# Kernel optimization log

Measured on AMD Instinct MI355X. Metric: run time of the kernel, lower is better.

The kernel has to match this reference:

```python
import jax, jax.numpy as jnp
import numpy as np

V, D, H, L, T_CTX = 50257, 768, 12, 12, 1024
HD = D // H
GELU_C = float(np.sqrt(2.0 / np.pi))


def new_gelu(x):
    return 0.5 * x * (1.0 + jnp.tanh(GELU_C * (x + 0.044715 * x ** 3)))


def layernorm(x, w, b, eps=1e-5):
    mu = jnp.mean(x, axis=-1, keepdims=True)
    var = jnp.var(x, axis=-1, keepdims=True)
    return (x - mu) * jax.lax.rsqrt(var + eps) * w + b


def setup_inputs() -> dict:
    key = jax.random.key(0)
    ks = jax.random.split(key, 20)
    B, T = 2, 1024
    s = 0.02
    inp = {
        "idx": jax.random.randint(ks[0], (B, T), 0, V),
        "targets": jax.random.randint(ks[1], (B, T), 0, V),
        "wte": jax.random.normal(ks[2], (V, D), jnp.float32) * s,
        "wpe": jax.random.normal(ks[3], (T_CTX, D), jnp.float32) * s,
        "ln1_w": jnp.ones((L, D)), "ln1_b": jnp.zeros((L, D)),
        "qkv_w": jax.random.normal(ks[4], (L, D, 3 * D), jnp.float32) * s,
        "qkv_b": jnp.zeros((L, 3 * D)),
        "proj_w": jax.random.normal(ks[5], (L, D, D), jnp.float32) * s,
        "proj_b": jnp.zeros((L, D)),
        "ln2_w": jnp.ones((L, D)), "ln2_b": jnp.zeros((L, D)),
        "fc_w": jax.random.normal(ks[6], (L, D, 4 * D), jnp.float32) * s,
        "fc_b": jnp.zeros((L, 4 * D)),
        "fc2_w": jax.random.normal(ks[7], (L, 4 * D, D), jnp.float32) * s,
        "fc2_b": jnp.zeros((L, D)),
        "lnf_w": jnp.ones((D,)), "lnf_b": jnp.zeros((D,)),
    }
    return inp


def _gpt_forward(idx, targets, wte, wpe, ln1_w, ln1_b, qkv_w, qkv_b, proj_w,
                 proj_b, ln2_w, ln2_b, fc_w, fc_b, fc2_w, fc2_b, lnf_w, lnf_b):
    B, T = idx.shape
    x = wte[idx] + wpe[:T]  # [B,T,D]
    scale = 1.0 / np.sqrt(HD)
    causal = jnp.tril(jnp.ones((T, T), dtype=bool))

    def block(x, p):
        l1w, l1b, qw, qb, pw, pb, l2w, l2b, fw, fb, f2w, f2b = p
        h = layernorm(x, l1w, l1b)
        qkv = h @ qw + qb  # [B,T,3D]
        q, k, v = jnp.split(qkv, 3, axis=-1)
        q = q.reshape(B, T, H, HD).transpose(0, 2, 1, 3)
        k = k.reshape(B, T, H, HD).transpose(0, 2, 1, 3)
        v = v.reshape(B, T, H, HD).transpose(0, 2, 1, 3)
        attn = jnp.einsum('bhqd,bhkd->bhqk', q, k) * scale
        attn = jnp.where(causal, attn, -jnp.inf)
        attn = jax.nn.softmax(attn, axis=-1)
        o = jnp.einsum('bhqk,bhkd->bhqd', attn, v)
        o = o.transpose(0, 2, 1, 3).reshape(B, T, D)
        x = x + (o @ pw + pb)
        h = layernorm(x, l2w, l2b)
        h = new_gelu(h @ fw + fb) @ f2w + f2b
        return x + h, None

    params = (ln1_w, ln1_b, qkv_w, qkv_b, proj_w, proj_b,
              ln2_w, ln2_b, fc_w, fc_b, fc2_w, fc2_b)
    x, _ = jax.lax.scan(block, x, params)
    x = layernorm(x, lnf_w, lnf_b)
    logits = x @ wte.T  # tied lm_head, [B,T,V]

    logp = jax.nn.log_softmax(logits, axis=-1)
    tflat = targets.reshape(-1)
    valid = tflat != -1
    tsafe = jnp.where(valid, tflat, 0)
    nll = -jnp.take_along_axis(logp.reshape(-1, V), tsafe[:, None], axis=-1)[:, 0]
    loss = jnp.sum(jnp.where(valid, nll, 0.0)) / jnp.maximum(jnp.sum(valid), 1)
    return logits, loss


def reference(idx, targets, wte, wpe, ln1_w, ln1_b, qkv_w, qkv_b, proj_w,
              proj_b, ln2_w, ln2_b, fc_w, fc_b, fc2_w, fc2_b, lnf_w, lnf_b):
    return _gpt_forward(idx, targets, wte, wpe, ln1_w, ln1_b, qkv_w, qkv_b,
                        proj_w, proj_b, ln2_w, ln2_b, fc_w, fc_b, fc2_w, fc2_b,
                        lnf_w, lnf_b)
```

## Files before the change

kernel.cpp:

```cpp
#include <hip/hip_runtime.h>
#include <hip/hip_bf16.h>
#include <math.h>

#define TT 1024
#define BB 2
#define DD 768
#define HH 12
#define NHD 64
#define LL 12
#define VV 50257
#define MROWS (BB*TT)
#define VPAD 50304

typedef __attribute__((ext_vector_type(4))) float f32x4;
typedef __attribute__((ext_vector_type(8))) __bf16 bf16x8;
typedef __attribute__((ext_vector_type(8))) unsigned short u16x8;
typedef __hip_bfloat16 bf16;

__device__ __forceinline__ void gload_lds16(const bf16* g, bf16* l) {
    __builtin_amdgcn_global_load_lds((const __attribute__((address_space(1))) void*)g,
                                     (__attribute__((address_space(3))) void*)l, 16, 0, 0);
}

__global__ void embed_kernel(const int* __restrict__ idx, const float* __restrict__ wte,
                             const float* __restrict__ wpe, float* __restrict__ x) {
    int m = blockIdx.x;
    int t = m % TT;
    int tok = idx[m];
    const float* wrow = wte + (size_t)tok * DD;
    const float* prow = wpe + (size_t)t * DD;
    float* xrow = x + (size_t)m * DD;
    for (int c = threadIdx.x; c < DD; c += blockDim.x)
        xrow[c] = wrow[c] + prow[c];
}

__global__ void ln_kernel(const float* __restrict__ x, const float* __restrict__ w,
                          const float* __restrict__ b, bf16* __restrict__ out) {
    __shared__ float red[256];
    int m = blockIdx.x;
    int tid = threadIdx.x;
    const float* xr = x + (size_t)m * DD;
    float v0 = xr[tid], v1 = xr[tid + 256], v2 = xr[tid + 512];
    red[tid] = v0 + v1 + v2;
    __syncthreads();
    for (int s = 128; s > 0; s >>= 1) { if (tid < s) red[tid] += red[tid + s]; __syncthreads(); }
    float mu = red[0] * (1.0f / DD);
    __syncthreads();
    float d0 = v0 - mu, d1 = v1 - mu, d2 = v2 - mu;
    red[tid] = d0 * d0 + d1 * d1 + d2 * d2;
    __syncthreads();
    for (int s = 128; s > 0; s >>= 1) { if (tid < s) red[tid] += red[tid + s]; __syncthreads(); }
    float rstd = rsqrtf(red[0] * (1.0f / DD) + 1e-5f);
    bf16* orow = out + (size_t)m * DD;
    orow[tid]       = __float2bfloat16(d0 * rstd * w[tid]       + b[tid]);
    orow[tid + 256] = __float2bfloat16(d1 * rstd * w[tid + 256] + b[tid + 256]);
    orow[tid + 512] = __float2bfloat16(d2 * rstd * w[tid + 512] + b[tid + 512]);
}

__global__ void cast_kernel(const float* __restrict__ src, bf16* __restrict__ dst, int n4) {
    int stride = gridDim.x * blockDim.x;
    for (int i = blockIdx.x * blockDim.x + threadIdx.x; i < n4; i += stride) {
        float4 v = *(const float4*)(src + (size_t)i * 4);
        bf16* d = dst + (size_t)i * 4;
        d[0] = __float2bfloat16(v.x); d[1] = __float2bfloat16(v.y);
        d[2] = __float2bfloat16(v.z); d[3] = __float2bfloat16(v.w);
    }
}

__global__ void tcast_kernel(const float* __restrict__ W, bf16* __restrict__ Wt,
                             int K, int N, size_t wstride, size_t tstride) {
    W  += (size_t)blockIdx.z * wstride;
    Wt += (size_t)blockIdx.z * tstride;
    __shared__ float t[32][33];
    int n0 = blockIdx.x * 32, k0 = blockIdx.y * 32;
    int c = threadIdx.x & 31, g = threadIdx.x >> 5;
    #pragma unroll
    for (int i = 0; i < 4; ++i) {
        int k = g * 4 + i;
        t[k][c] = W[(size_t)(k0 + k) * N + n0 + c];
    }
    __syncthreads();
    #pragma unroll
    for (int i = 0; i < 4; ++i) {
        int n = g * 4 + i;
        Wt[(size_t)(n0 + n) * K + k0 + c] = __float2bfloat16(t[c][n]);
    }
}

template<int BM, int BN, bool BIAS, bool GELU_, bool RES, bool OUTBF16, bool NCHECK>
__global__ __launch_bounds__(256, 3) void mgemm(
        const bf16* __restrict__ A, const bf16* __restrict__ Bm,
        const float* __restrict__ bias, const float* __restrict__ res,
        float* __restrict__ Cf, bf16* __restrict__ Cb, int M, int N, int K) {
    constexpr int WM = BM / 32, WN = BN / 32;
    constexpr int RA = BM / 64, RB = BN / 64;
    constexpr int NL = RA + RB;
    __shared__ __align__(16) bf16 As[3][BM * 32];
    __shared__ __align__(16) bf16 Bs[3][BN * 32];
    const int tid = threadIdx.x, lane = tid & 63, wid = tid >> 6;
    const int nbx = gridDim.x;
    const int nwg = nbx * gridDim.y;
    const int bidl = blockIdx.x + nbx * blockIdx.y;
    const int cpx = nwg >> 3;
    const int sw = (bidl & 7) * cpx + (bidl >> 3);
    const int m0 = (sw % nbx) * BM, n0 = (sw / nbx) * BN;
    const int wr = (wid >> 1) * (BM / 2), wc = (wid & 1) * (BN / 2);
    const int fr = lane & 15, fq = lane >> 4;

    const int ksrc = ((lane & 3) ^ ((lane >> 3) & 3)) * 8;
    const bf16* gA = A  + (size_t)(m0 + wid * 16 + (lane >> 2)) * K + ksrc;
    const bf16* gB = Bm + (size_t)(n0 + wid * 16 + (lane >> 2)) * K + ksrc;
    const int kph = (fq ^ ((fr >> 1) & 3)) * 8;

    const int nt = K / 32;
    auto stage = [&](int tile) {
        bf16* dA = &As[tile % 3][0] + wid * 512 + lane * 8;
        bf16* dB = &Bs[tile % 3][0] + wid * 512 + lane * 8;
        const bf16* pA = gA + tile * 32;
        const bf16* pB = gB + tile * 32;
        #pragma unroll
        for (int i = 0; i < RA; ++i) gload_lds16(pA + (size_t)(i * 64) * K, dA + i * 2048);
        #pragma unroll
        for (int i = 0; i < RB; ++i) gload_lds16(pB + (size_t)(i * 64) * K, dB + i * 2048);
    };

    f32x4 acc[WM][WN] = {};
    stage(0);
    if (nt > 1) stage(1);

    for (int t = 0; t < nt; ++t) {
        if (t + 2 < nt) stage(t + 2);
        const int rem = nt - 1 - t;
        if (rem >= 2)      asm volatile("s_waitcnt vmcnt(%0)" :: "i"(2 * NL) : "memory");
        else if (rem == 1) asm volatile("s_waitcnt vmcnt(%0)" :: "i"(NL) : "memory");
        else               asm volatile("s_waitcnt vmcnt(0)" ::: "memory");
        __builtin_amdgcn_s_barrier();
        __builtin_amdgcn_sched_barrier(0);
        const bf16* abase = &As[t % 3][0];
        const bf16* bbase = &Bs[t % 3][0];
        bf16x8 af[WM], bq[WN];
        #pragma unroll
        for (int m = 0; m < WM; ++m)
            af[m] = *(const bf16x8*)(abase + (wr + m * 16 + fr) * 32 + kph);
        #pragma unroll
        for (int n = 0; n < WN; ++n)
            bq[n] = *(const bf16x8*)(bbase + (wc + n * 16 + fr) * 32 + kph);
        #pragma unroll
        for (int m = 0; m < WM; ++m)
            #pragma unroll
            for (int n = 0; n < WN; ++n)
                acc[m][n] = __builtin_amdgcn_mfma_f32_16x16x32_bf16(af[m], bq[n], acc[m][n], 0, 0, 0);
        __builtin_amdgcn_sched_barrier(0);
        __builtin_amdgcn_s_barrier();
    }

    #pragma unroll
    for (int m = 0; m < WM; ++m) {
        const int row = m0 + wr + m * 16 + fq * 4;
        #pragma unroll
        for (int n = 0; n < WN; ++n) {
            const int col = n0 + wc + n * 16 + fr;
            if (NCHECK && col >= N) continue;
            float bv = BIAS ? bias[col] : 0.f;
            #pragma unroll
            for (int r = 0; r < 4; ++r) {
                float v = acc[m][n][r] + bv;
                if (GELU_) {
                    float u = v;
                    v = 0.5f * u * (1.0f + tanhf(0.7978845608028654f * (u + 0.044715f * u * u * u)));
                }
                if (RES) v += res[(size_t)(row + r) * N + col];
                if (OUTBF16) Cb[(size_t)(row + r) * N + col] = __float2bfloat16(v);
                else         Cf[(size_t)(row + r) * N + col] = v;
            }
        }
    }
}

__global__ __launch_bounds__(256) void attn3_kernel(const bf16* __restrict__ qkv,
                                                    bf16* __restrict__ out) {
    __shared__ bf16 Vt[64 * 64];
    __shared__ bf16 Ps[4][16 * 64];
    const int bid = blockIdx.x;
    const int q0 = (bid % (TT / 64)) * 64;
    const int h  = (bid / (TT / 64)) % HH;
    const int b  = bid / ((TT / 64) * HH);
    const int tid = threadIdx.x, lane = tid & 63, wid = tid >> 6;
    const int fr = lane & 15, fq = lane >> 4;
    const size_t rs = 3 * DD;

    bf16x8 qf[2];
    {
        const bf16* qb = qkv + (size_t)(b * TT + q0 + wid * 16 + fr) * rs + h * NHD;
        qf[0] = *(const bf16x8*)(qb + fq * 8);
        qf[1] = *(const bf16x8*)(qb + 32 + fq * 8);
    }
    float mrun[4] = {-1e30f, -1e30f, -1e30f, -1e30f};
    float lrun[4] = {0.f, 0.f, 0.f, 0.f};
    f32x4 o[4] = {};
    const int vrow = (tid & 31) * 2, kq = tid >> 5;
    const int ntile = q0 / 64 + 1;

    for (int jt = 0; jt < ntile; ++jt) {
        __syncthreads();
        {
            const u16x8* vb = (const u16x8*)(qkv + (size_t)(b * TT + jt * 64 + vrow) * rs + 2 * DD + h * NHD + kq * 8);
            u16x8 v0 = vb[0];
            u16x8 v1 = *(const u16x8*)((const bf16*)vb + rs);
            #pragma unroll
            for (int j = 0; j < 8; ++j) {
                int d = kq * 8 + j;
                int e = (d * 64 + vrow) ^ ((d & 7) << 3);
                *(unsigned int*)&Vt[e] = (unsigned int)v0[j] | ((unsigned int)v1[j] << 16);
            }
        }
        f32x4 s[4] = {};
        const bf16* kb = qkv + (size_t)(b * TT + jt * 64 + fr) * rs + DD + h * NHD;
        #pragma unroll
        for (int n = 0; n < 4; ++n) {
            bf16x8 k0 = *(const bf16x8*)(kb + (size_t)(n * 16) * rs + fq * 8);
            bf16x8 k1 = *(const bf16x8*)(kb + (size_t)(n * 16) * rs + 32 + fq * 8);
            s[n] = __builtin_amdgcn_mfma_f32_16x16x32_bf16(qf[0], k0, s[n], 0, 0, 0);
            s[n] = __builtin_amdgcn_mfma_f32_16x16x32_bf16(qf[1], k1, s[n], 0, 0, 0);
        }
        float mt[4] = {-1e30f, -1e30f, -1e30f, -1e30f};
        #pragma unroll
        for (int n = 0; n < 4; ++n) {
            int colg = jt * 64 + n * 16 + fr;
            #pragma unroll
            for (int r = 0; r < 4; ++r) {
                int rowg = q0 + wid * 16 + fq * 4 + r;
                float v = s[n][r] * 0.125f;
                if (colg > rowg) v = -1e30f;
                s[n][r] = v;
                mt[r] = fmaxf(mt[r], v);
            }
        }
        #pragma unroll
        for (int msk = 1; msk <= 8; msk <<= 1)
            #pragma unroll
            for (int r = 0; r < 4; ++r) mt[r] = fmaxf(mt[r], __shfl_xor(mt[r], msk));
        float sc[4], pt[4] = {0.f, 0.f, 0.f, 0.f};
        #pragma unroll
        for (int r = 0; r < 4; ++r) {
            float mn = fmaxf(mrun[r], mt[r]);
            sc[r] = __expf(mrun[r] - mn);
            mrun[r] = mn;
        }
        #pragma unroll
        for (int n = 0; n < 4; ++n)
            #pragma unroll
            for (int r = 0; r < 4; ++r) {
                float p = __expf(s[n][r] - mrun[r]);
                s[n][r] = p;
                pt[r] += p;
            }
        #pragma unroll
        for (int msk = 1; msk <= 8; msk <<= 1)
            #pragma unroll
            for (int r = 0; r < 4; ++r) pt[r] += __shfl_xor(pt[r], msk);
        #pragma unroll
        for (int r = 0; r < 4; ++r) lrun[r] = lrun[r] * sc[r] + pt[r];
        #pragma unroll
        for (int n2 = 0; n2 < 4; ++n2)
            #pragma unroll
            for (int r = 0; r < 4; ++r) o[n2][r] *= sc[r];
        #pragma unroll
        for (int n = 0; n < 4; ++n)
            #pragma unroll
            for (int r = 0; r < 4; ++r) {
                int row = fq * 4 + r;
                int e = (row * 64 + n * 16 + fr) ^ ((row & 7) << 3);
                Ps[wid][e] = __float2bfloat16(s[n][r]);
            }
        __syncthreads();
        #pragma unroll
        for (int ks = 0; ks < 2; ++ks) {
            int pe = (fr * 64 + ks * 32 + fq * 8) ^ ((fr & 7) << 3);
            bf16x8 pa = *(const bf16x8*)&Ps[wid][pe];
            #pragma unroll
            for (int n2 = 0; n2 < 4; ++n2) {
                int d = n2 * 16 + fr;
                int ve = (d * 64 + ks * 32 + fq * 8) ^ ((d & 7) << 3);
                bf16x8 vv = *(const bf16x8*)&Vt[ve];
                o[n2] = __builtin_amdgcn_mfma_f32_16x16x32_bf16(pa, vv, o[n2], 0, 0, 0);
            }
        }
    }
    #pragma unroll
    for (int r = 0; r < 4; ++r) {
        float inv = 1.f / lrun[r];
        bf16* op = out + (size_t)(b * TT + q0 + wid * 16 + fq * 4 + r) * DD + h * NHD;
        #pragma unroll
        for (int n2 = 0; n2 < 4; ++n2)
            op[n2 * 16 + fr] = __float2bfloat16(o[n2][r] * inv);
    }
}

__global__ void zero_kernel(float* p) { if (threadIdx.x == 0) p[0] = 0.f; }

__device__ __forceinline__ void ol_push(float v, float& mx, float& sm) {
    if (v > mx) { sm *= __expf(mx - v); mx = v; }
    sm += __expf(v - mx);
}

__global__ void loss_kernel(const float* __restrict__ logits, const int* __restrict__ targets,
                            float* __restrict__ acc) {
    __shared__ float rm[256], rs[256];
    int m = blockIdx.x;
    int tid = threadIdx.x;
    const float* lr = logits + (size_t)m * VV;
    const int lead = (4 - (m & 3)) & 3;
    const int nv = (VV - lead) >> 2;
    float mx = -1e30f, sm = 0.f;
    if (tid < lead) ol_push(lr[tid], mx, sm);
    const float4* lr4 = (const float4*)(lr + lead);
    for (int i = tid; i < nv; i += 256) {
        float4 v = lr4[i];
        ol_push(v.x, mx, sm); ol_push(v.y, mx, sm);
        ol_push(v.z, mx, sm); ol_push(v.w, mx, sm);
    }
    for (int i = lead + 4 * nv + tid; i < VV; i += 256) ol_push(lr[i], mx, sm);
    rm[tid] = mx; rs[tid] = sm;
    __syncthreads();
    for (int s = 128; s > 0; s >>= 1) {
        if (tid < s) {
            float m2 = rm[tid + s], s2 = rs[tid + s];
            float nm = fmaxf(rm[tid], m2);
            rs[tid] = rs[tid] * __expf(rm[tid] - nm) + s2 * __expf(m2 - nm);
            rm[tid] = nm;
        }
        __syncthreads();
    }
    if (tid == 0) {
        float lse = logf(rs[0]) + rm[0];
        atomicAdd(acc, lse - lr[targets[m]]);
    }
}

__global__ void loss_final(const float* __restrict__ acc, float* __restrict__ out) {
    if (threadIdx.x == 0) out[0] = acc[0] * (1.0f / (float)MROWS);
}

extern "C" void kernel_launch(void* const* d_in, const int* in_sizes, int n_in,
                              void* d_out, int out_size, void* d_ws, size_t ws_size,
                              hipStream_t stream) {
    const int*   idx     = (const int*)d_in[0];
    const int*   targets = (const int*)d_in[1];
    const float* wte     = (const float*)d_in[2];
    const float* wpe     = (const float*)d_in[3];
    const float* ln1_w   = (const float*)d_in[4];
    const float* ln1_b   = (const float*)d_in[5];
    const float* qkv_w   = (const float*)d_in[6];
    const float* qkv_b   = (const float*)d_in[7];
    const float* proj_w  = (const float*)d_in[8];
    const float* proj_b  = (const float*)d_in[9];
    const float* ln2_w   = (const float*)d_in[10];
    const float* ln2_b   = (const float*)d_in[11];
    const float* fc_w    = (const float*)d_in[12];
    const float* fc_b    = (const float*)d_in[13];
    const float* fc2_w   = (const float*)d_in[14];
    const float* fc2_b   = (const float*)d_in[15];
    const float* lnf_w   = (const float*)d_in[16];
    const float* lnf_b   = (const float*)d_in[17];

    float* logits = (float*)d_out;
    float* loss_out = logits + (size_t)MROWS * VV;

    const size_t LQ = (size_t)3 * DD * DD, LP = (size_t)DD * DD;
    const size_t LF = (size_t)4 * DD * DD, LF2 = (size_t)4 * DD * DD;
    const size_t LSTRIDE = LQ + LP + LF + LF2;

    float* x    = (float*)d_ws;
    float* lacc = x + (size_t)MROWS * DD;
    bf16* qkvbuf = (bf16*)(lacc + 16);
    bf16* hb   = qkvbuf + (size_t)MROWS * 3 * DD;
    bf16* ab   = hb + (size_t)MROWS * DD;
    bf16* gb   = ab + (size_t)MROWS * DD;
    bf16* wteb = gb + (size_t)MROWS * 4 * DD;
    bf16* wbase = wteb + (size_t)VPAD * DD;

    const size_t fixed_bytes = (size_t)((char*)wbase - (char*)d_ws);
    const bool hoist = ws_size >= fixed_bytes + sizeof(bf16) * LSTRIDE * LL;

    dim3 blk(256);
    cast_kernel<<<2048, blk, 0, stream>>>(wte, wteb, VV * DD / 4);
    embed_kernel<<<MROWS, blk, 0, stream>>>(idx, wte, wpe, x);

    if (hoist) {
        tcast_kernel<<<dim3(3 * DD / 32, DD / 32, LL), blk, 0, stream>>>(
            qkv_w, wbase, DD, 3 * DD, LQ, LSTRIDE);
        tcast_kernel<<<dim3(DD / 32, DD / 32, LL), blk, 0, stream>>>(
            proj_w, wbase + LQ, DD, DD, LP, LSTRIDE);
        tcast_kernel<<<dim3(4 * DD / 32, DD / 32, LL), blk, 0, stream>>>(
            fc_w, wbase + LQ + LP, DD, 4 * DD, LF, LSTRIDE);
        tcast_kernel<<<dim3(DD / 32, 4 * DD / 32, LL), blk, 0, stream>>>(
            fc2_w, wbase + LQ + LP + LF, 4 * DD, DD, LF2, LSTRIDE);
    }

    for (int l = 0; l < LL; ++l) {
        bf16* wl = hoist ? wbase + (size_t)l * LSTRIDE : wbase;
        bf16* wQT = wl, *wPT = wl + LQ, *wFT = wl + LQ + LP, *wF2T = wl + LQ + LP + LF;
        if (!hoist) {
            tcast_kernel<<<dim3(3 * DD / 32, DD / 32, 1), blk, 0, stream>>>(qkv_w + (size_t)l * LQ, wQT, DD, 3 * DD, 0, 0);
            tcast_kernel<<<dim3(DD / 32, DD / 32, 1), blk, 0, stream>>>(proj_w + (size_t)l * LP, wPT, DD, DD, 0, 0);
            tcast_kernel<<<dim3(4 * DD / 32, DD / 32, 1), blk, 0, stream>>>(fc_w + (size_t)l * LF, wFT, DD, 4 * DD, 0, 0);
            tcast_kernel<<<dim3(DD / 32, 4 * DD / 32, 1), blk, 0, stream>>>(fc2_w + (size_t)l * LF2, wF2T, 4 * DD, DD, 0, 0);
        }

        ln_kernel<<<MROWS, blk, 0, stream>>>(x, ln1_w + (size_t)l * DD, ln1_b + (size_t)l * DD, hb);

        mgemm<128, 128, true, false, false, true, false><<<dim3(MROWS / 128, 3 * DD / 128), blk, 0, stream>>>(
            hb, wQT, qkv_b + (size_t)l * 3 * DD, nullptr, nullptr, qkvbuf, MROWS, 3 * DD, DD);

        attn3_kernel<<<BB * HH * (TT / 64), blk, 0, stream>>>(qkvbuf, ab);

        mgemm<64, 64, true, false, true, false, false><<<dim3(MROWS / 64, DD / 64), blk, 0, stream>>>(
            ab, wPT, proj_b + (size_t)l * DD, x, x, nullptr, MROWS, DD, DD);

        ln_kernel<<<MROWS, blk, 0, stream>>>(x, ln2_w + (size_t)l * DD, ln2_b + (size_t)l * DD, hb);

        mgemm<128, 128, true, true, false, true, false><<<dim3(MROWS / 128, 4 * DD / 128), blk, 0, stream>>>(
            hb, wFT, fc_b + (size_t)l * 4 * DD, nullptr, nullptr, gb, MROWS, 4 * DD, DD);

        mgemm<64, 64, true, false, true, false, false><<<dim3(MROWS / 64, DD / 64), blk, 0, stream>>>(
            gb, wF2T, fc2_b + (size_t)l * DD, x, x, nullptr, MROWS, DD, 4 * DD);
    }

    ln_kernel<<<MROWS, blk, 0, stream>>>(x, lnf_w, lnf_b, hb);

    mgemm<128, 128, false, false, false, false, true><<<dim3(MROWS / 128, VPAD / 128), blk, 0, stream>>>(
        hb, wteb, nullptr, nullptr, logits, nullptr, MROWS, VV, DD);

    zero_kernel<<<1, 64, 0, stream>>>(lacc);
    loss_kernel<<<MROWS, blk, 0, stream>>>(logits, targets, lacc);
    loss_final<<<1, 64, 0, stream>>>(lacc, loss_out);
}
```

Before: 2.600 ms.

## Split-K the residual GEMMs, double-buffer mgemm, reorder attention blocks with setprio

The proj and fc2 GEMMs now split K across two z-slices that write fp32 partials, and a new reduction kernel adds the partials, bias and residual into x. This raises the workgroup count for the small N=768 GEMMs. The mgemm pipeline drops from three LDS stages to two, which cuts LDS use but makes load/compute overlap shallower for every GEMM, including the large lm_head GEMM. Attention blocks are launched longest-causal-first, and s_setprio is raised around MFMA sections. Together these add an extra kernel launch per residual GEMM and extra fp32 partial traffic.

```diff
diff --git a/kernel.cpp b/kernel.cpp
--- a/kernel.cpp
+++ b/kernel.cpp
@@ -87,7 +87,7 @@
     }
 }
 
-template<int BM, int BN, bool BIAS, bool GELU_, bool RES, bool OUTBF16, bool NCHECK>
+template<int BM, int BN, bool BIAS, bool GELU_, bool RES, bool OUTBF16, bool NCHECK, bool SPLITK>
 __global__ __launch_bounds__(256, 3) void mgemm(
         const bf16* __restrict__ A, const bf16* __restrict__ Bm,
         const float* __restrict__ bias, const float* __restrict__ res,
@@ -95,8 +95,8 @@
     constexpr int WM = BM / 32, WN = BN / 32;
     constexpr int RA = BM / 64, RB = BN / 64;
     constexpr int NL = RA + RB;
-    __shared__ __align__(16) bf16 As[3][BM * 32];
-    __shared__ __align__(16) bf16 Bs[3][BN * 32];
+    __shared__ __align__(16) bf16 As[2][BM * 32];
+    __shared__ __align__(16) bf16 Bs[2][BN * 32];
     const int tid = threadIdx.x, lane = tid & 63, wid = tid >> 6;
     const int nbx = gridDim.x;
     const int nwg = nbx * gridDim.y;
@@ -107,37 +107,44 @@
     const int wr = (wid >> 1) * (BM / 2), wc = (wid & 1) * (BN / 2);
     const int fr = lane & 15, fq = lane >> 4;
 
+    const int Keff  = SPLITK ? (K >> 1) : K;
+    const int kbase = SPLITK ? blockIdx.z * Keff : 0;
+    if (SPLITK) Cf += (size_t)blockIdx.z * M * N;
+
     const int ksrc = ((lane & 3) ^ ((lane >> 3) & 3)) * 8;
-    const bf16* gA = A  + (size_t)(m0 + wid * 16 + (lane >> 2)) * K + ksrc;
-    const bf16* gB = Bm + (size_t)(n0 + wid * 16 + (lane >> 2)) * K + ksrc;
+    const bf16* gA = A  + (size_t)(m0 + wid * 16 + (lane >> 2)) * K + kbase + ksrc;
+    const bf16* gB = Bm + (size_t)(n0 + wid * 16 + (lane >> 2)) * K + kbase + ksrc;
+    bf16* lA = &As[0][0] + wid * 512 + lane * 8;
+    bf16* lB = &Bs[0][0] + wid * 512 + lane * 8;
     const int kph = (fq ^ ((fr >> 1) & 3)) * 8;
 
-    const int nt = K / 32;
-    auto stage = [&](int tile) {
-        bf16* dA = &As[tile % 3][0] + wid * 512 + lane * 8;
-        bf16* dB = &Bs[tile % 3][0] + wid * 512 + lane * 8;
-        const bf16* pA = gA + tile * 32;
-        const bf16* pB = gB + tile * 32;
-        #pragma unroll
-        for (int i = 0; i < RA; ++i) gload_lds16(pA + (size_t)(i * 64) * K, dA + i * 2048);
-        #pragma unroll
-        for (int i = 0; i < RB; ++i) gload_lds16(pB + (size_t)(i * 64) * K, dB + i * 2048);
-    };
-
     f32x4 acc[WM][WN] = {};
-    stage(0);
-    if (nt > 1) stage(1);
+    const int nt = Keff / 32;
+
+    #pragma unroll
+    for (int i = 0; i < RA; ++i) gload_lds16(gA + (size_t)(i * 64) * K, lA + i * 2048);
+    #pragma unroll
+    for (int i = 0; i < RB; ++i) gload_lds16(gB + (size_t)(i * 64) * K, lB + i * 2048);
 
     for (int t = 0; t < nt; ++t) {
-        if (t + 2 < nt) stage(t + 2);
-        const int rem = nt - 1 - t;
-        if (rem >= 2)      asm volatile("s_waitcnt vmcnt(%0)" :: "i"(2 * NL) : "memory");
-        else if (rem == 1) asm volatile("s_waitcnt vmcnt(%0)" :: "i"(NL) : "memory");
-        else               asm volatile("s_waitcnt vmcnt(0)" ::: "memory");
+        const int cur = t & 1;
+        if (t + 1 < nt) {
+            const bf16* pA = gA + (t + 1) * 32;
+            const bf16* pB = gB + (t + 1) * 32;
+            bf16* dA = lA + (cur ^ 1) * (BM * 32);
+            bf16* dB = lB + (cur ^ 1) * (BN * 32);
+            #pragma unroll
+            for (int i = 0; i < RA; ++i) gload_lds16(pA + (size_t)(i * 64) * K, dA + i * 2048);
+            #pragma unroll
+            for (int i = 0; i < RB; ++i) gload_lds16(pB + (size_t)(i * 64) * K, dB + i * 2048);
+            asm volatile("s_waitcnt vmcnt(%0)" :: "i"(NL) : "memory");
+        } else {
+            asm volatile("s_waitcnt vmcnt(0)" ::: "memory");
+        }
         __builtin_amdgcn_s_barrier();
         __builtin_amdgcn_sched_barrier(0);
-        const bf16* abase = &As[t % 3][0];
-        const bf16* bbase = &Bs[t % 3][0];
+        const bf16* abase = &As[cur][0];
+        const bf16* bbase = &Bs[cur][0];
         bf16x8 af[WM], bq[WN];
         #pragma unroll
         for (int m = 0; m < WM; ++m)
@@ -177,12 +184,27 @@
     }
 }
 
+__global__ void red_kernel(const float* __restrict__ part, const float* __restrict__ bias,
+                           float* __restrict__ x) {
+    const size_t MN = (size_t)MROWS * DD;
+    size_t i = ((size_t)blockIdx.x * blockDim.x + threadIdx.x) * 4;
+    float4 p0 = *(const float4*)(part + i);
+    float4 p1 = *(const float4*)(part + MN + i);
+    float4 xv = *(const float4*)(x + i);
+    float4 bv = *(const float4*)(bias + (int)(i % DD));
+    xv.x += p0.x + p1.x + bv.x;
+    xv.y += p0.y + p1.y + bv.y;
+    xv.z += p0.z + p1.z + bv.z;
+    xv.w += p0.w + p1.w + bv.w;
+    *(float4*)(x + i) = xv;
+}
+
 __global__ __launch_bounds__(256) void attn3_kernel(const bf16* __restrict__ qkv,
                                                     bf16* __restrict__ out) {
     __shared__ bf16 Vt[64 * 64];
     __shared__ bf16 Ps[4][16 * 64];
     const int bid = blockIdx.x;
-    const int q0 = (bid % (TT / 64)) * 64;
+    const int q0 = (15 - (bid & 15)) * 64;
     const int h  = (bid / (TT / 64)) % HH;
     const int b  = bid / ((TT / 64) * HH);
     const int tid = threadIdx.x, lane = tid & 63, wid = tid >> 6;
@@ -216,6 +238,7 @@
         }
         f32x4 s[4] = {};
         const bf16* kb = qkv + (size_t)(b * TT + jt * 64 + fr) * rs + DD + h * NHD;
+        __builtin_amdgcn_s_setprio(1);
         #pragma unroll
         for (int n = 0; n < 4; ++n) {
             bf16x8 k0 = *(const bf16x8*)(kb + (size_t)(n * 16) * rs + fq * 8);
@@ -223,6 +246,7 @@
             s[n] = __builtin_amdgcn_mfma_f32_16x16x32_bf16(qf[0], k0, s[n], 0, 0, 0);
             s[n] = __builtin_amdgcn_mfma_f32_16x16x32_bf16(qf[1], k1, s[n], 0, 0, 0);
         }
+        __builtin_amdgcn_s_setprio(0);
         float mt[4] = {-1e30f, -1e30f, -1e30f, -1e30f};
         #pragma unroll
         for (int n = 0; n < 4; ++n) {
@@ -274,6 +298,7 @@
                 Ps[wid][e] = __float2bfloat16(s[n][r]);
             }
         __syncthreads();
+        __builtin_amdgcn_s_setprio(1);
         #pragma unroll
         for (int ks = 0; ks < 2; ++ks) {
             int pe = (fr * 64 + ks * 32 + fq * 8) ^ ((fr & 7) << 3);
@@ -286,6 +311,7 @@
                 o[n2] = __builtin_amdgcn_mfma_f32_16x16x32_bf16(pa, vv, o[n2], 0, 0, 0);
             }
         }
+        __builtin_amdgcn_s_setprio(0);
     }
     #pragma unroll
     for (int r = 0; r < 4; ++r) {
@@ -373,7 +399,8 @@
 
     float* x    = (float*)d_ws;
     float* lacc = x + (size_t)MROWS * DD;
-    bf16* qkvbuf = (bf16*)(lacc + 16);
+    float* part = lacc + 16;
+    bf16* qkvbuf = (bf16*)(part + (size_t)2 * MROWS * DD);
     bf16* hb   = qkvbuf + (size_t)MROWS * 3 * DD;
     bf16* ab   = hb + (size_t)MROWS * DD;
     bf16* gb   = ab + (size_t)MROWS * DD;
@@ -398,6 +425,8 @@
             fc2_w, wbase + LQ + LP + LF, 4 * DD, DD, LF2, LSTRIDE);
     }
 
+    const int nred = (MROWS * DD) / (4 * 256);
+
     for (int l = 0; l < LL; ++l) {
         bf16* wl = hoist ? wbase + (size_t)l * LSTRIDE : wbase;
         bf16* wQT = wl, *wPT = wl + LQ, *wFT = wl + LQ + LP, *wF2T = wl + LQ + LP + LF;
@@ -410,26 +439,28 @@
 
         ln_kernel<<<MROWS, blk, 0, stream>>>(x, ln1_w + (size_t)l * DD, ln1_b + (size_t)l * DD, hb);
 
-        mgemm<128, 128, true, false, false, true, false><<<dim3(MROWS / 128, 3 * DD / 128), blk, 0, stream>>>(
+        mgemm<128, 128, true, false, false, true, false, false><<<dim3(MROWS / 128, 3 * DD / 128), blk, 0, stream>>>(
             hb, wQT, qkv_b + (size_t)l * 3 * DD, nullptr, nullptr, qkvbuf, MROWS, 3 * DD, DD);
 
         attn3_kernel<<<BB * HH * (TT / 64), blk, 0, stream>>>(qkvbuf, ab);
 
-        mgemm<64, 64, true, false, true, false, false><<<dim3(MROWS / 64, DD / 64), blk, 0, stream>>>(
-            ab, wPT, proj_b + (size_t)l * DD, x, x, nullptr, MROWS, DD, DD);
+        mgemm<64, 64, false, false, false, false, false, true><<<dim3(MROWS / 64, DD / 64, 2), blk, 0, stream>>>(
+            ab, wPT, nullptr, nullptr, part, nullptr, MROWS, DD, DD);
+        red_kernel<<<nred, blk, 0, stream>>>(part, proj_b + (size_t)l * DD, x);
 
         ln_kernel<<<MROWS, blk, 0, stream>>>(x, ln2_w + (size_t)l * DD, ln2_b + (size_t)l * DD, hb);
 
-        mgemm<128, 128, true, true, false, true, false><<<dim3(MROWS / 128, 4 * DD / 128), blk, 0, stream>>>(
+        mgemm<128, 128, true, true, false, true, false, false><<<dim3(MROWS / 128, 4 * DD / 128), blk, 0, stream>>>(
             hb, wFT, fc_b + (size_t)l * 4 * DD, nullptr, nullptr, gb, MROWS, 4 * DD, DD);
 
-        mgemm<64, 64, true, false, true, false, false><<<dim3(MROWS / 64, DD / 64), blk, 0, stream>>>(
-            gb, wF2T, fc2_b + (size_t)l * DD, x, x, nullptr, MROWS, DD, 4 * DD);
+        mgemm<64, 64, false, false, false, false, false, true><<<dim3(MROWS / 64, DD / 64, 2), blk, 0, stream>>>(
+            gb, wF2T, nullptr, nullptr, part, nullptr, MROWS, DD, 4 * DD);
+        red_kernel<<<nred, blk, 0, stream>>>(part, fc2_b + (size_t)l * DD, x);
     }
 
     ln_kernel<<<MROWS, blk, 0, stream>>>(x, lnf_w, lnf_b, hb);
 
-    mgemm<128, 128, false, false, false, false, true><<<dim3(MROWS / 128, VPAD / 128), blk, 0, stream>>>(
+    mgemm<128, 128, false, false, false, false, true, false><<<dim3(MROWS / 128, VPAD / 128), blk, 0, stream>>>(
         hb, wteb, nullptr, nullptr, logits, nullptr, MROWS, VV, DD);
 
     zero_kernel<<<1, 64, 0, stream>>>(lacc);
```

Result: no change. 2.567 ms (-1.3%).
